# Kernel tuning notes

Hardware: AMD Instinct MI355X
Metric: run time of the kernel (lower is better)

Reference implementation:

```python
import jax, jax.numpy as jnp
import numpy as np

INPUT_DIM = 2048
EMBED_DIM = 128


def setup_inputs() -> dict:
    key = jax.random.key(0)
    kx, kw, kb, kv = jax.random.split(key, 4)
    x = jax.random.normal(kx, (16384, INPUT_DIM), dtype=jnp.float32)
    # nn.Linear(input_dim, 1): weight [1, D] (init std=0.01), bias [1]
    W = jax.random.normal(kw, (1, INPUT_DIM), dtype=jnp.float32) * 0.01
    b = jax.random.normal(kb, (1,), dtype=jnp.float32) * 0.01
    # nn.Embedding(input_dim, embedding_dim): V [D, K] (init std=0.01)
    V = jax.random.normal(kv, (INPUT_DIM, EMBED_DIM), dtype=jnp.float32) * 0.01
    return {"x": x, "W": W, "b": b, "V": V}


def reference(x, W, b, V):
    # linear part: x @ W^T + b -> [B, 1]
    linear_part = x @ W.T + b
    # FM 2nd-order interaction via the standard identity:
    # 0.5 * sum_k ( (sum_d x_d V_dk)^2 - sum_d x_d^2 V_dk^2 )
    # equals the original sum_square - square_sum over weighted embeddings.
    xv = x @ V                       # [B, K]
    x2v2 = (x * x) @ (V * V)         # [B, K]
    interaction = 0.5 * jnp.sum(xv * xv - x2v2, axis=1, keepdims=True)
    return linear_part + interaction
```

## Files before the change

### kernel.cpp

```cpp
#include <hip/hip_runtime.h>
#include <hip/hip_bf16.h>

#define INPUT_DIM 2048
#define EMBED_DIM 128
#define NROWS 16384

typedef __bf16 bf16x8 __attribute__((ext_vector_type(8)));
typedef float f32x4 __attribute__((ext_vector_type(4)));

__device__ inline float dot4(f32x4 a, f32x4 b) {
    return a.x * b.x + a.y * b.y + a.z * b.z + a.w * b.w;
}

__global__ __launch_bounds__(256) void fm_prep(const float* __restrict__ V,
                                               __bf16* __restrict__ Vt,
                                               float* __restrict__ s) {
    __shared__ float tile[64][132];
    const int t = threadIdx.x;
    const int k0 = blockIdx.x * 64;

#pragma unroll
    for (int i = 0; i < 8; ++i) {
        int idx = i * 256 + t;
        int kk = idx >> 5;
        int nq = (idx & 31) * 4;
        *(f32x4*)&tile[kk][nq] = *(const f32x4*)(V + (size_t)(k0 + kk) * EMBED_DIM + nq);
    }
    __syncthreads();

    {
        const int n = t >> 1;
        const int ks = (t & 1) * 32;
        __bf16 ov[32];
#pragma unroll
        for (int j = 0; j < 32; ++j) ov[j] = (__bf16)tile[ks + j][n];
#pragma unroll
        for (int q = 0; q < 4; ++q)
            *(bf16x8*)(Vt + (size_t)n * INPUT_DIM + k0 + ks + q * 8) = *(bf16x8*)&ov[q * 8];
    }

    if (t < 64) {
        float a = 0.f;
#pragma unroll
        for (int n4 = 0; n4 < 32; ++n4) {
            f32x4 v = *(f32x4*)&tile[t][n4 * 4];
            a += dot4(v, v);
        }
        s[k0 + t] = a;
    }
}

__global__ __launch_bounds__(256, 3) void fm_main(const float* __restrict__ x,
                                                  const float* __restrict__ W,
                                                  const float* __restrict__ bptr,
                                                  const __bf16* __restrict__ Vt,
                                                  const float* __restrict__ s,
                                                  float* __restrict__ out) {
    __shared__ __align__(16) float acc_lds[4][16][132];
    __shared__ float lin_lds[4][16];
    __shared__ float sq_lds[4][16];

    const int tid = threadIdx.x;
    const int w = tid >> 6;
    const int l = tid & 63;
    const int lr = l & 15;
    const int lg = l >> 4;

    const int row0 = blockIdx.x * 16;
    const int k0 = w * 512;

    const float* xp = x + (size_t)(row0 + lr) * INPUT_DIM + k0 + lg * 8;
    const float* wp = W + k0 + lg * 8;
    const float* sp = s + k0 + lg * 8;
    const __bf16* vtp = Vt + (size_t)lr * INPUT_DIM + k0 + lg * 8;

    f32x4 acc[8];
#pragma unroll
    for (int c = 0; c < 8; ++c) acc[c] = (f32x4){0.f, 0.f, 0.f, 0.f};
    float lin = 0.f, sq = 0.f;

    f32x4 ca0 = *(const f32x4*)xp;
    f32x4 ca1 = *(const f32x4*)(xp + 4);

#pragma unroll 4
    for (int step = 0; step < 16; ++step) {
        f32x4 na0 = ca0, na1 = ca1;
        if (step < 15) {
            na0 = *(const f32x4*)(xp + 32);
            na1 = *(const f32x4*)(xp + 36);
        }
        bf16x8 vb0 = *(const bf16x8*)(vtp + 0 * 16 * INPUT_DIM);
        bf16x8 vb1 = *(const bf16x8*)(vtp + 1 * 16 * INPUT_DIM);
        bf16x8 vb2 = *(const bf16x8*)(vtp + 2 * 16 * INPUT_DIM);
        bf16x8 vb3 = *(const bf16x8*)(vtp + 3 * 16 * INPUT_DIM);
        bf16x8 vb4 = *(const bf16x8*)(vtp + 4 * 16 * INPUT_DIM);
        bf16x8 vb5 = *(const bf16x8*)(vtp + 5 * 16 * INPUT_DIM);
        bf16x8 vb6 = *(const bf16x8*)(vtp + 6 * 16 * INPUT_DIM);
        bf16x8 vb7 = *(const bf16x8*)(vtp + 7 * 16 * INPUT_DIM);
        f32x4 w0 = *(const f32x4*)wp;
        f32x4 w1 = *(const f32x4*)(wp + 4);
        f32x4 s0 = *(const f32x4*)sp;
        f32x4 s1 = *(const f32x4*)(sp + 4);

        lin += dot4(ca0, w0) + dot4(ca1, w1);
        sq += dot4(ca0 * ca0, s0) + dot4(ca1 * ca1, s1);

        bf16x8 af;
        af[0] = (__bf16)ca0.x; af[1] = (__bf16)ca0.y;
        af[2] = (__bf16)ca0.z; af[3] = (__bf16)ca0.w;
        af[4] = (__bf16)ca1.x; af[5] = (__bf16)ca1.y;
        af[6] = (__bf16)ca1.z; af[7] = (__bf16)ca1.w;

        acc[0] = __builtin_amdgcn_mfma_f32_16x16x32_bf16(af, vb0, acc[0], 0, 0, 0);
        acc[1] = __builtin_amdgcn_mfma_f32_16x16x32_bf16(af, vb1, acc[1], 0, 0, 0);
        acc[2] = __builtin_amdgcn_mfma_f32_16x16x32_bf16(af, vb2, acc[2], 0, 0, 0);
        acc[3] = __builtin_amdgcn_mfma_f32_16x16x32_bf16(af, vb3, acc[3], 0, 0, 0);
        acc[4] = __builtin_amdgcn_mfma_f32_16x16x32_bf16(af, vb4, acc[4], 0, 0, 0);
        acc[5] = __builtin_amdgcn_mfma_f32_16x16x32_bf16(af, vb5, acc[5], 0, 0, 0);
        acc[6] = __builtin_amdgcn_mfma_f32_16x16x32_bf16(af, vb6, acc[6], 0, 0, 0);
        acc[7] = __builtin_amdgcn_mfma_f32_16x16x32_bf16(af, vb7, acc[7], 0, 0, 0);

        ca0 = na0; ca1 = na1;
        xp += 32; wp += 32; sp += 32; vtp += 32;
    }

#pragma unroll
    for (int c = 0; c < 8; ++c)
#pragma unroll
        for (int r = 0; r < 4; ++r)
            acc_lds[w][lg * 4 + r][c * 16 + lr] = acc[c][r];

    lin += __shfl_xor(lin, 16); lin += __shfl_xor(lin, 32);
    sq  += __shfl_xor(sq, 16);  sq  += __shfl_xor(sq, 32);
    if (l < 16) { lin_lds[w][l] = lin; sq_lds[w][l] = sq; }
    __syncthreads();

    {
        const int row = tid >> 4;
        const int nc = (tid & 15) * 8;
        f32x4 v0 = (f32x4){0.f, 0.f, 0.f, 0.f};
        f32x4 v1 = (f32x4){0.f, 0.f, 0.f, 0.f};
#pragma unroll
        for (int ww = 0; ww < 4; ++ww) {
            v0 += *(const f32x4*)&acc_lds[ww][row][nc];
            v1 += *(const f32x4*)&acc_lds[ww][row][nc + 4];
        }
        float ss = dot4(v0, v0) + dot4(v1, v1);
        ss += __shfl_xor(ss, 1);
        ss += __shfl_xor(ss, 2);
        ss += __shfl_xor(ss, 4);
        ss += __shfl_xor(ss, 8);
        if ((tid & 15) == 0) {
            float linf = lin_lds[0][row] + lin_lds[1][row] + lin_lds[2][row] + lin_lds[3][row];
            float sqf  = sq_lds[0][row] + sq_lds[1][row] + sq_lds[2][row] + sq_lds[3][row];
            out[row0 + row] = linf + bptr[0] + 0.5f * (ss - sqf);
        }
    }
}

extern "C" void kernel_launch(void* const* d_in, const int* in_sizes, int n_in,
                              void* d_out, int out_size, void* d_ws, size_t ws_size,
                              hipStream_t stream) {
    const float* x = (const float*)d_in[0];
    const float* W = (const float*)d_in[1];
    const float* b = (const float*)d_in[2];
    const float* V = (const float*)d_in[3];
    float* out = (float*)d_out;

    __bf16* Vt = (__bf16*)d_ws;
    float* s = (float*)((char*)d_ws + 128 * 2048 * sizeof(__bf16));

    fm_prep<<<32, 256, 0, stream>>>(V, Vt, s);
    fm_main<<<1024, 256, 0, stream>>>(x, W, b, Vt, s, out);
}
```

Measured before the change: 250.5 us.

## Stage x and V tiles through double-buffered LDS with direct global-to-LDS loads

The main kernel now processes 64 rows per block with 512 threads. Four waves issue global_load_lds copies of x tiles and four copy pre-swizzled V tiles into double-buffered LDS, and all eight waves run MFMAs from LDS. The prep kernel now writes V in per-k-chunk XOR-swizzled blocks so LDS reads avoid bank conflicts, and W and s are staged once in LDS. The aim is to overlap the next tile's loads with compute and to stop every wave reloading V from global memory. In exchange the grid shrinks to 256 blocks, at most one per CU, and each tile ends in a block-wide barrier, which may limit memory parallelism.

Result: faster. 204.8 us (-18.2%).

```diff
diff --git a/kernel.cpp b/kernel.cpp
--- a/kernel.cpp
+++ b/kernel.cpp
@@ -1,160 +1,214 @@
 #include <hip/hip_runtime.h>
 #include <hip/hip_bf16.h>
 
-#define INPUT_DIM 2048
-#define EMBED_DIM 128
-#define NROWS 16384
+#define K_DIM 2048
+#define N_DIM 128
+#define BM 64
+#define BK 64
+#define NTILES (K_DIM / BK)
+#define VT_CHUNK 16384
 
 typedef __bf16 bf16x8 __attribute__((ext_vector_type(8)));
 typedef float f32x4 __attribute__((ext_vector_type(4)));
 
-__device__ inline float dot4(f32x4 a, f32x4 b) {
+__device__ __forceinline__ float dot4(f32x4 a, f32x4 b) {
     return a.x * b.x + a.y * b.y + a.z * b.z + a.w * b.w;
 }
 
+__device__ __forceinline__ void gload16(const void* g, void* lds) {
+    __builtin_amdgcn_global_load_lds(
+        (const __attribute__((address_space(1))) unsigned int*)g,
+        (__attribute__((address_space(3))) unsigned int*)lds,
+        16, 0, 0);
+}
+
 __global__ __launch_bounds__(256) void fm_prep(const float* __restrict__ V,
-                                               __bf16* __restrict__ Vt,
+                                               char* __restrict__ VtS,
                                                float* __restrict__ s) {
     __shared__ float tile[64][132];
     const int t = threadIdx.x;
-    const int k0 = blockIdx.x * 64;
-
+    const int kb = blockIdx.x;
+    const int k0 = kb * 64;
 #pragma unroll
     for (int i = 0; i < 8; ++i) {
         int idx = i * 256 + t;
         int kk = idx >> 5;
         int nq = (idx & 31) * 4;
-        *(f32x4*)&tile[kk][nq] = *(const f32x4*)(V + (size_t)(k0 + kk) * EMBED_DIM + nq);
+        *(f32x4*)&tile[kk][nq] = *(const f32x4*)(V + (size_t)(k0 + kk) * N_DIM + nq);
     }
     __syncthreads();
-
     {
         const int n = t >> 1;
-        const int ks = (t & 1) * 32;
-        __bf16 ov[32];
-#pragma unroll
-        for (int j = 0; j < 32; ++j) ov[j] = (__bf16)tile[ks + j][n];
-#pragma unroll
-        for (int q = 0; q < 4; ++q)
-            *(bf16x8*)(Vt + (size_t)n * INPUT_DIM + k0 + ks + q * 8) = *(bf16x8*)&ov[q * 8];
-    }
-
+        const int half = t & 1;
+        const int sw = (n & 7) << 4;
+        char* dstbase = VtS + (size_t)kb * VT_CHUNK + n * 128;
+#pragma unroll
+        for (int g = 0; g < 4; ++g) {
+            int kkg = half * 32 + g * 8;
+            bf16x8 o;
+#pragma unroll
+            for (int e = 0; e < 8; ++e) o[e] = (__bf16)tile[kkg + e][n];
+            *(bf16x8*)(dstbase + ((kkg * 2) ^ sw)) = o;
+        }
+    }
     if (t < 64) {
         float a = 0.f;
 #pragma unroll
-        for (int n4 = 0; n4 < 32; ++n4) {
-            f32x4 v = *(f32x4*)&tile[t][n4 * 4];
+        for (int nq = 0; nq < 32; ++nq) {
+            f32x4 v = *(f32x4*)&tile[t][nq * 4];
             a += dot4(v, v);
         }
         s[k0 + t] = a;
     }
 }
 
-__global__ __launch_bounds__(256, 3) void fm_main(const float* __restrict__ x,
+__global__ __launch_bounds__(512, 2) void fm_main(const float* __restrict__ x,
                                                   const float* __restrict__ W,
                                                   const float* __restrict__ bptr,
-                                                  const __bf16* __restrict__ Vt,
+                                                  const char* __restrict__ VtS,
                                                   const float* __restrict__ s,
                                                   float* __restrict__ out) {
-    __shared__ __align__(16) float acc_lds[4][16][132];
+    __shared__ __align__(16) char xbuf[2][16384];
+    __shared__ __align__(16) char vbuf[2][16384];
+    __shared__ __align__(16) float Wl[2048];
+    __shared__ __align__(16) float Sl[2048];
     __shared__ float lin_lds[4][16];
     __shared__ float sq_lds[4][16];
+    __shared__ float ss_lds[4][2][16];
 
     const int tid = threadIdx.x;
     const int w = tid >> 6;
     const int l = tid & 63;
     const int lr = l & 15;
     const int lg = l >> 4;
-
-    const int row0 = blockIdx.x * 16;
-    const int k0 = w * 512;
-
-    const float* xp = x + (size_t)(row0 + lr) * INPUT_DIM + k0 + lg * 8;
-    const float* wp = W + k0 + lg * 8;
-    const float* sp = s + k0 + lg * 8;
-    const __bf16* vtp = Vt + (size_t)lr * INPUT_DIM + k0 + lg * 8;
-
-    f32x4 acc[8];
-#pragma unroll
-    for (int c = 0; c < 8; ++c) acc[c] = (f32x4){0.f, 0.f, 0.f, 0.f};
+    const int wr = w >> 1;
+    const int wc = w & 1;
+    const int row0 = blockIdx.x * BM;
+
+    *(f32x4*)&Wl[tid * 4] = *(const f32x4*)(W + tid * 4);
+    *(f32x4*)&Sl[tid * 4] = *(const f32x4*)(s + tid * 4);
+
+    const bool isX = (w < 4);
+    const char* src[4];
+    int loff[4];
+    if (isX) {
+#pragma unroll
+        for (int j = 0; j < 4; ++j) {
+            int gi = w * 4 + j;
+            int rowt = gi * 4 + lg;
+            int koff = (lr * 16) ^ ((rowt & 7) << 4);
+            src[j] = (const char*)x + (size_t)(row0 + rowt) * (K_DIM * 4) + koff;
+            loff[j] = gi * 1024;
+        }
+    } else {
+#pragma unroll
+        for (int j = 0; j < 4; ++j) {
+            int vi = (w - 4) * 4 + j;
+            src[j] = VtS + vi * 1024 + l * 16;
+            loff[j] = vi * 1024;
+        }
+    }
+
+    f32x4 acc[4];
+#pragma unroll
+    for (int c = 0; c < 4; ++c) acc[c] = (f32x4){0.f, 0.f, 0.f, 0.f};
     float lin = 0.f, sq = 0.f;
 
-    f32x4 ca0 = *(const f32x4*)xp;
-    f32x4 ca1 = *(const f32x4*)(xp + 4);
-
-#pragma unroll 4
-    for (int step = 0; step < 16; ++step) {
-        f32x4 na0 = ca0, na1 = ca1;
-        if (step < 15) {
-            na0 = *(const f32x4*)(xp + 32);
-            na1 = *(const f32x4*)(xp + 36);
-        }
-        bf16x8 vb0 = *(const bf16x8*)(vtp + 0 * 16 * INPUT_DIM);
-        bf16x8 vb1 = *(const bf16x8*)(vtp + 1 * 16 * INPUT_DIM);
-        bf16x8 vb2 = *(const bf16x8*)(vtp + 2 * 16 * INPUT_DIM);
-        bf16x8 vb3 = *(const bf16x8*)(vtp + 3 * 16 * INPUT_DIM);
-        bf16x8 vb4 = *(const bf16x8*)(vtp + 4 * 16 * INPUT_DIM);
-        bf16x8 vb5 = *(const bf16x8*)(vtp + 5 * 16 * INPUT_DIM);
-        bf16x8 vb6 = *(const bf16x8*)(vtp + 6 * 16 * INPUT_DIM);
-        bf16x8 vb7 = *(const bf16x8*)(vtp + 7 * 16 * INPUT_DIM);
-        f32x4 w0 = *(const f32x4*)wp;
-        f32x4 w1 = *(const f32x4*)(wp + 4);
-        f32x4 s0 = *(const f32x4*)sp;
-        f32x4 s1 = *(const f32x4*)(sp + 4);
-
-        lin += dot4(ca0, w0) + dot4(ca1, w1);
-        sq += dot4(ca0 * ca0, s0) + dot4(ca1 * ca1, s1);
-
-        bf16x8 af;
-        af[0] = (__bf16)ca0.x; af[1] = (__bf16)ca0.y;
-        af[2] = (__bf16)ca0.z; af[3] = (__bf16)ca0.w;
-        af[4] = (__bf16)ca1.x; af[5] = (__bf16)ca1.y;
-        af[6] = (__bf16)ca1.z; af[7] = (__bf16)ca1.w;
-
-        acc[0] = __builtin_amdgcn_mfma_f32_16x16x32_bf16(af, vb0, acc[0], 0, 0, 0);
-        acc[1] = __builtin_amdgcn_mfma_f32_16x16x32_bf16(af, vb1, acc[1], 0, 0, 0);
-        acc[2] = __builtin_amdgcn_mfma_f32_16x16x32_bf16(af, vb2, acc[2], 0, 0, 0);
-        acc[3] = __builtin_amdgcn_mfma_f32_16x16x32_bf16(af, vb3, acc[3], 0, 0, 0);
-        acc[4] = __builtin_amdgcn_mfma_f32_16x16x32_bf16(af, vb4, acc[4], 0, 0, 0);
-        acc[5] = __builtin_amdgcn_mfma_f32_16x16x32_bf16(af, vb5, acc[5], 0, 0, 0);
-        acc[6] = __builtin_amdgcn_mfma_f32_16x16x32_bf16(af, vb6, acc[6], 0, 0, 0);
-        acc[7] = __builtin_amdgcn_mfma_f32_16x16x32_bf16(af, vb7, acc[7], 0, 0, 0);
-
-        ca0 = na0; ca1 = na1;
-        xp += 32; wp += 32; sp += 32; vtp += 32;
-    }
-
-#pragma unroll
-    for (int c = 0; c < 8; ++c)
-#pragma unroll
-        for (int r = 0; r < 4; ++r)
-            acc_lds[w][lg * 4 + r][c * 16 + lr] = acc[c][r];
-
-    lin += __shfl_xor(lin, 16); lin += __shfl_xor(lin, 32);
-    sq  += __shfl_xor(sq, 16);  sq  += __shfl_xor(sq, 32);
-    if (l < 16) { lin_lds[w][l] = lin; sq_lds[w][l] = sq; }
+    if (isX) {
+#pragma unroll
+        for (int j = 0; j < 4; ++j) gload16(src[j], &xbuf[0][loff[j]]);
+    } else {
+#pragma unroll
+        for (int j = 0; j < 4; ++j) gload16(src[j], &vbuf[0][loff[j]]);
+    }
     __syncthreads();
 
-    {
-        const int row = tid >> 4;
-        const int nc = (tid & 15) * 8;
-        f32x4 v0 = (f32x4){0.f, 0.f, 0.f, 0.f};
-        f32x4 v1 = (f32x4){0.f, 0.f, 0.f, 0.f};
-#pragma unroll
-        for (int ww = 0; ww < 4; ++ww) {
-            v0 += *(const f32x4*)&acc_lds[ww][row][nc];
-            v1 += *(const f32x4*)&acc_lds[ww][row][nc + 4];
-        }
-        float ss = dot4(v0, v0) + dot4(v1, v1);
-        ss += __shfl_xor(ss, 1);
-        ss += __shfl_xor(ss, 2);
-        ss += __shfl_xor(ss, 4);
-        ss += __shfl_xor(ss, 8);
-        if ((tid & 15) == 0) {
-            float linf = lin_lds[0][row] + lin_lds[1][row] + lin_lds[2][row] + lin_lds[3][row];
-            float sqf  = sq_lds[0][row] + sq_lds[1][row] + sq_lds[2][row] + sq_lds[3][row];
-            out[row0 + row] = linf + bptr[0] + 0.5f * (ss - sqf);
-        }
+    const int rowt = wr * 16 + lr;
+    const int swA = (rowt & 7) << 4;
+    const char* arowbase = &xbuf[0][0] + rowt * 256;
+
+    for (int t = 0; t < NTILES; ++t) {
+        const int cur = t & 1;
+        if (t < NTILES - 1) {
+            if (isX) {
+#pragma unroll
+                for (int j = 0; j < 4; ++j)
+                    gload16(src[j] + (size_t)(t + 1) * (BK * 4), &xbuf[cur ^ 1][loff[j]]);
+            } else {
+#pragma unroll
+                for (int j = 0; j < 4; ++j)
+                    gload16(src[j] + (size_t)(t + 1) * VT_CHUNK, &vbuf[cur ^ 1][loff[j]]);
+            }
+        }
+
+        const char* arow = &xbuf[cur][0] + rowt * 256;
+        const char* vb = &vbuf[cur][0];
+
+        bf16x8 af[2];
+        f32x4 alo[2], ahi[2];
+#pragma unroll
+        for (int kb = 0; kb < 2; ++kb) {
+            const int kA = kb * 128 + lg * 32;
+            alo[kb] = *(const f32x4*)(arow + (kA ^ swA));
+            ahi[kb] = *(const f32x4*)(arow + ((kA + 16) ^ swA));
+            af[kb][0] = (__bf16)alo[kb].x; af[kb][1] = (__bf16)alo[kb].y;
+            af[kb][2] = (__bf16)alo[kb].z; af[kb][3] = (__bf16)alo[kb].w;
+            af[kb][4] = (__bf16)ahi[kb].x; af[kb][5] = (__bf16)ahi[kb].y;
+            af[kb][6] = (__bf16)ahi[kb].z; af[kb][7] = (__bf16)ahi[kb].w;
+        }
+        if (wc == 0) {
+            const int ki = t * 64 + lg * 8;
+#pragma unroll
+            for (int kb = 0; kb < 2; ++kb) {
+                f32x4 w0 = *(const f32x4*)&Wl[ki + kb * 32];
+                f32x4 w1 = *(const f32x4*)&Wl[ki + kb * 32 + 4];
+                f32x4 s0 = *(const f32x4*)&Sl[ki + kb * 32];
+                f32x4 s1 = *(const f32x4*)&Sl[ki + kb * 32 + 4];
+                lin += dot4(alo[kb], w0) + dot4(ahi[kb], w1);
+                sq  += dot4(alo[kb] * alo[kb], s0) + dot4(ahi[kb] * ahi[kb], s1);
+            }
+        }
+#pragma unroll
+        for (int c = 0; c < 4; ++c) {
+            const int nt = wc * 64 + c * 16 + lr;
+            const int swB = (nt & 7) << 4;
+            const char* brow = vb + nt * 128;
+#pragma unroll
+            for (int kb = 0; kb < 2; ++kb) {
+                bf16x8 bf = *(const bf16x8*)(brow + ((kb * 64 + lg * 16) ^ swB));
+                acc[c] = __builtin_amdgcn_mfma_f32_16x16x32_bf16(af[kb], bf, acc[c], 0, 0, 0);
+            }
+        }
+        __syncthreads();
+    }
+    (void)arowbase;
+
+    f32x4 vss = (f32x4){0.f, 0.f, 0.f, 0.f};
+#pragma unroll
+    for (int c = 0; c < 4; ++c) vss += acc[c] * acc[c];
+#pragma unroll
+    for (int m = 1; m < 16; m <<= 1) {
+        vss.x += __shfl_xor(vss.x, m);
+        vss.y += __shfl_xor(vss.y, m);
+        vss.z += __shfl_xor(vss.z, m);
+        vss.w += __shfl_xor(vss.w, m);
+    }
+    if (lr == 0) {
+        ss_lds[wr][wc][lg * 4 + 0] = vss.x;
+        ss_lds[wr][wc][lg * 4 + 1] = vss.y;
+        ss_lds[wr][wc][lg * 4 + 2] = vss.z;
+        ss_lds[wr][wc][lg * 4 + 3] = vss.w;
+    }
+    if (wc == 0) {
+        lin += __shfl_xor(lin, 16); lin += __shfl_xor(lin, 32);
+        sq  += __shfl_xor(sq, 16);  sq  += __shfl_xor(sq, 32);
+        if (l < 16) { lin_lds[wr][l] = lin; sq_lds[wr][l] = sq; }
+    }
+    __syncthreads();
+    if (tid < 64) {
+        const int wrI = tid >> 4, r16 = tid & 15;
+        out[row0 + tid] = lin_lds[wrI][r16] + bptr[0]
+            + 0.5f * (ss_lds[wrI][0][r16] + ss_lds[wrI][1][r16] - sq_lds[wrI][r16]);
     }
 }
 
@@ -167,9 +221,9 @@
     const float* V = (const float*)d_in[3];
     float* out = (float*)d_out;
 
-    __bf16* Vt = (__bf16*)d_ws;
-    float* s = (float*)((char*)d_ws + 128 * 2048 * sizeof(__bf16));
-
-    fm_prep<<<32, 256, 0, stream>>>(V, Vt, s);
-    fm_main<<<1024, 256, 0, stream>>>(x, W, b, Vt, s, out);
-}
+    char* VtS = (char*)d_ws;
+    float* s = (float*)((char*)d_ws + 32 * VT_CHUNK);
+
+    fm_prep<<<32, 256, 0, stream>>>(V, VtS, s);
+    fm_main<<<256, 512, 0, stream>>>(x, W, b, VtS, s, out);
+}
```
